# Kernel tuning notes

Hardware: AMD Instinct MI355X
Metric: run time of the kernel (lower is better)

## Reference

```python
import jax, jax.numpy as jnp
import numpy as np

BINS = np.array([1, 2, 3, 4, 8, 16, 32, 64], dtype=np.int32)


def setup_inputs() -> dict:
    N, G, F, H, K = 1024, 620, 20, 150, 128
    D_in = 3 * G + F  # 1880
    key = jax.random.key(0)
    ks = jax.random.split(key, 10)
    g = jax.random.normal(ks[0], (N, G), dtype=jnp.float32)
    si = jax.random.normal(ks[1], (N,), dtype=jnp.float32)
    i1 = jnp.sort(jax.random.randint(ks[2], (N,), 0, 8192)).astype(jnp.int32)
    i2 = jnp.sort(jax.random.randint(ks[3], (N,), 0, 8192)).astype(jnp.int32)
    dist_emb = jax.random.normal(ks[4], (9, F), dtype=jnp.float32) * 0.02
    W1 = jax.random.normal(ks[5], (D_in, H), dtype=jnp.float32) * (1.0 / np.sqrt(D_in))
    b1 = jnp.zeros((H,), jnp.float32)
    W2 = jax.random.normal(ks[6], (H, H), dtype=jnp.float32) * (1.0 / np.sqrt(H))
    b2 = jnp.zeros((H,), jnp.float32)
    W3 = jax.random.normal(ks[7], (H, 1), dtype=jnp.float32) * (1.0 / np.sqrt(H))
    b3 = jnp.zeros((1,), jnp.float32)
    return {"g": g, "si": si, "i1": i1, "i2": i2, "dist_emb": dist_emb,
            "W1": W1, "b1": b1, "W2": W2, "b2": b2, "W3": W3, "b3": b3, "K": K}


def reference(g, si, i1, i2, dist_emb, W1, b1, W2, b2, W3, b3, K):
    # Dropout is inference-disabled; epsilon dummy antecedent appended as last column.
    N, G = g.shape
    # span n's antecedents are spans [max(0, n-K), n); lay out as [N, K] window
    j_idx = jnp.arange(N)[:, None] - K + jnp.arange(K)[None, :]  # [N, K]
    valid = j_idx >= 0
    j = jnp.clip(j_idx, 0, N - 1)
    g_j = g[j]                      # [N, K, G] ragged gather (masked dense)
    g_i = g[:, None, :]             # [N, 1, G]
    # distance feature: bin(i.i2 - j.i1) with idx = #bins <= d
    d = i2[:, None] - i1[j]         # [N, K]
    bin_idx = jnp.searchsorted(jnp.asarray(BINS), d, side='right')
    de = dist_emb[bin_idx]          # [N, K, F]
    pairs = jnp.concatenate(
        [jnp.broadcast_to(g_i, (N, K, G)), g_j, g_i * g_j, de], axis=-1)  # [N, K, 3G+F]
    h = jax.nn.relu(jnp.einsum('nkd,dh->nkh', pairs, W1) + b1)
    h = jax.nn.relu(jnp.einsum('nkh,hm->nkm', h, W2) + b2)
    s = (jnp.einsum('nkh,ho->nko', h, W3) + b3)[..., 0]  # [N, K]
    sij = si[:, None] + si[j] + s
    sij = jnp.where(valid, sij, 0.0)
    eps = jnp.zeros((N, 1), sij.dtype)  # epsilon dummy score
    return jnp.concatenate([sij, eps], axis=-1)  # [N, K+1]
```

## Files before the change

kernel.cpp:

```cpp
#include <hip/hip_runtime.h>
#include <hip/hip_bf16.h>
#include <stdint.h>

typedef __attribute__((ext_vector_type(8))) short short8;
typedef __attribute__((ext_vector_type(4))) float float4_t;

#define N_PTS 1024
#define G_DIM 620
#define G_PAD 640
#define F_DIM 20
#define H_DIM 150
#define H_PAD 160
#define K_WIN 128
#define OUT_C (K_WIN + 1)

__device__ __forceinline__ float bf2f(short u) {
  union { unsigned int i; float f; } x;
  x.i = ((unsigned int)(unsigned short)u) << 16;
  return x.f;
}
__device__ __forceinline__ short f2bf(float f) {
  union { float f; unsigned int i; } x; x.f = f;
  unsigned int u = x.i;
  u += 0x7FFFu + ((u >> 16) & 1u);
  return (short)(u >> 16);
}
__device__ __forceinline__ short f2bf_hw(float f) {
  __hip_bfloat16 h = __float2bfloat16(f);
  union { __hip_bfloat16 h; short s; } u; u.h = h;
  return u.s;
}
__device__ __forceinline__ void gload_lds16(const void* g, void* l) {
  __builtin_amdgcn_global_load_lds(
      (const __attribute__((address_space(1))) unsigned int*)g,
      (__attribute__((address_space(3))) unsigned int*)l, 16, 0, 0);
}

__global__ void prep_pack(const float* __restrict__ g, const float* __restrict__ W1,
                          const float* __restrict__ W2, const float* __restrict__ dist_emb,
                          short* __restrict__ g_bf, short* __restrict__ W1cT,
                          short* __restrict__ W1abT, short* __restrict__ W2T,
                          float* __restrict__ deW) {
  __shared__ float lds[32 * 165];
  const int bx = blockIdx.x, tid = threadIdx.x;
  if (bx < 256) {
    const int n0 = bx * 4;
    for (int c = tid; c < 320; c += 256) {
      int r = c / 80, cc = c - r * 80;
      int n = n0 + r, d0 = cc * 8;
      short8 o;
      if (d0 + 8 <= G_DIM) {
        const float* src = g + n * G_DIM + d0;
        #pragma unroll
        for (int e = 0; e < 8; ++e) o[e] = f2bf(src[e]);
      } else {
        #pragma unroll
        for (int e = 0; e < 8; ++e) {
          int d = d0 + e;
          o[e] = (d < G_DIM) ? f2bf(g[n * G_DIM + d]) : (short)0;
        }
      }
      *(short8*)(g_bf + n * G_PAD + d0) = o;
    }
  } else if (bx < 316) {
    const int tb = bx - 256;
    const int third = tb / 20, dt = tb - third * 20;
    const int d0 = dt * 32;
    for (int c = tid; c < 1280; c += 256) {
      int dr = c / 40, ch4 = c - dr * 40;
      int dd = d0 + dr;
      int w1r = third * G_DIM + dd;
      #pragma unroll
      for (int e = 0; e < 4; ++e) {
        int h = ch4 * 4 + e;
        lds[dr * 165 + h] = (dd < G_DIM && h < H_DIM) ? W1[w1r * H_DIM + h] : 0.f;
      }
    }
    __syncthreads();
    short* outp = (third == 2) ? W1cT : (W1abT + third * H_PAD * G_PAD);
    for (int c = tid; c < 640; c += 256) {
      int h = c >> 2, ch = c & 3;
      short8 o;
      #pragma unroll
      for (int e = 0; e < 8; ++e) o[e] = f2bf(lds[(ch * 8 + e) * 165 + h]);
      *(short8*)(outp + h * G_PAD + d0 + ch * 8) = o;
    }
  } else if (bx < 320) {
    const int base = (bx - 316) * 6400;
    for (int c = tid; c < 6400; c += 256) {
      int q = base + c;
      int m = q / H_PAD, k = q - m * H_PAD;
      W2T[q] = (m < H_DIM && k < H_DIM) ? f2bf(W2[k * H_DIM + m]) : (short)0;
    }
  } else {
    for (int c = tid; c < 9 * H_PAD; c += 256) {
      int b = c / H_PAD, h = c - b * H_PAD;
      float acc = 0.f;
      if (h < H_DIM)
        for (int f = 0; f < F_DIM; ++f)
          acc += dist_emb[b * F_DIM + f] * W1[(3 * G_DIM + f) * H_DIM + h];
      deW[c] = acc;
    }
  }
}

__global__ __launch_bounds__(256) void prep_uv_mfma(
    const short* __restrict__ g_bf, const short* __restrict__ W1abT,
    const float* __restrict__ b1, float* __restrict__ U, float* __restrict__ V) {
  __shared__ __align__(16) char sA[32 * 128];
  __shared__ __align__(16) char sB[160 * 128];
  const int m0 = blockIdx.x * 32;
  const int yb = blockIdx.y * H_PAD;
  const int tid = threadIdx.x, lane = tid & 63, wid = tid >> 6;
  const int wm = wid >> 1, wn = wid & 1;
  const int lo4 = lane & 15, hi2 = lane >> 4;
  const int l8 = lane >> 3, c8 = lane & 7;
  const int xe = (c8 ^ (l8 & 7)) * 8;

  const float4_t fz = {0.f, 0.f, 0.f, 0.f};
  float4_t acc[5];
  #pragma unroll
  for (int b = 0; b < 5; ++b) acc[b] = fz;

  for (int step = 0; step < 10; ++step) {
    const int d0 = step * 64;
    {
      int row = wid * 8 + l8;
      gload_lds16(g_bf + (m0 + row) * G_PAD + d0 + xe, sA + (wid * 8) * 128);
    }
    #pragma unroll
    for (int cc = 0; cc < 5; ++cc) {
      int row = wid * 8 + cc * 32 + l8;
      gload_lds16(W1abT + (yb + row) * G_PAD + d0 + xe, sB + (wid * 8 + cc * 32) * 128);
    }
    __syncthreads();
    #pragma unroll
    for (int ks = 0; ks < 2; ++ks) {
      const int kb = ks * 64 + 16 * hi2;
      short8 af, bq[5];
      {
        int row = wm * 16 + lo4;
        af = *((const short8*)(sA + row * 128 + (kb ^ ((row & 7) << 4))));
      }
      #pragma unroll
      for (int nt = 0; nt < 5; ++nt) {
        int row = wn * 80 + nt * 16 + lo4;
        bq[nt] = *((const short8*)(sB + row * 128 + (kb ^ ((row & 7) << 4))));
      }
      #pragma unroll
      for (int nt = 0; nt < 5; ++nt)
        acc[nt] = __builtin_amdgcn_mfma_f32_16x16x32_bf16(af, bq[nt], acc[nt], 0, 0, 0);
    }
    __syncthreads();
  }

  const bool isU = (blockIdx.y == 0);
  float* O = isU ? U : V;
  #pragma unroll
  for (int r = 0; r < 4; ++r) {
    int m = m0 + wm * 16 + hi2 * 4 + r;
    #pragma unroll
    for (int nt = 0; nt < 5; ++nt) {
      int h = wn * 80 + nt * 16 + lo4;
      float v = acc[nt][r];
      if (h < H_DIM) { if (isU) v += b1[h]; } else { v = 0.f; }
      O[m * H_PAD + h] = v;
    }
  }
}

__global__ __launch_bounds__(512, 4) void pair_main(
    const short* __restrict__ g_bf, const short* __restrict__ W1cT,
    const short* __restrict__ W2T, const float* __restrict__ U,
    const float* __restrict__ V, const float* __restrict__ deW,
    const float* __restrict__ si, const int* __restrict__ i1,
    const int* __restrict__ i2, const float* __restrict__ W3,
    const float* __restrict__ b2, const float* __restrict__ b3,
    float* __restrict__ out) {
  __shared__ __align__(16) char smem[73728];
  __shared__ __align__(16) short gi_s[G_PAD];
  __shared__ float sj_s[K_WIN];
  __shared__ unsigned char bin_su[K_WIN];
  __shared__ float s_buf[2][K_WIN];

  char* const P0 = smem;
  char* const P1 = smem + 16384;
  char* const B0 = smem + 32768;
  char* const B1 = smem + 53248;
  char* const Hb = smem;

  const int bid = blockIdx.x;
  const int i = ((bid & 7) << 7) | (bid >> 3);
  const int tid = threadIdx.x;
  const int lane = tid & 63;
  const int wid = tid >> 6;
  const int wm = wid >> 1;
  const int wn = wid & 1;
  const int lo4 = lane & 15, hi2 = lane >> 4;
  const int l8 = lane >> 3, c8 = lane & 7;
  const int xe = (c8 ^ (l8 & 7)) * 8;
  const int tc8 = tid & 7;

  if (tid < G_PAD / 8)
    ((short8*)gi_s)[tid] = ((const short8*)(g_bf + i * G_PAD))[tid];
  if (tid < K_WIN) {
    int jr = i - K_WIN + tid, jc = jr < 0 ? 0 : jr;
    int d = i2[i] - i1[jc];
    bin_su[tid] = (unsigned char)((d >= 1) + (d >= 2) + (d >= 3) + (d >= 4) +
                                  (d >= 8) + (d >= 16) + (d >= 32) + (d >= 64));
    sj_s[tid] = si[jc];
  }
  __syncthreads();

  auto loadA = [&](int s, short8 (&gjv)[2], short8& gvv) {
    const int d0 = s * 64;
    gvv = *((const short8*)(gi_s + d0 + tc8 * 8));
    #pragma unroll
    for (int cc = 0; cc < 2; ++cc) {
      int c = tid + 512 * cc, row = c >> 3;
      int jr = i - K_WIN + row, jc = jr < 0 ? 0 : jr;
      gjv[cc] = *((const short8*)(g_bf + jc * G_PAD + d0 + tc8 * 8));
    }
  };
  auto stageB = [&](int s, char* B) {
    const int d0 = s * 64;
    #pragma unroll
    for (int cc = 0; cc < 3; ++cc) {
      if (cc < 2 || wid < 4) {
        int rowb = wid * 8 + cc * 64;
        gload_lds16(W1cT + (rowb + l8) * G_PAD + d0 + xe, B + rowb * 128);
      }
    }
  };
  auto writeP = [&](char* P, const short8 (&gjv)[2], const short8& gvv) {
    #pragma unroll
    for (int cc = 0; cc < 2; ++cc) {
      int c = tid + 512 * cc, row = c >> 3;
      short8 p;
      #pragma unroll
      for (int e = 0; e < 8; ++e) p[e] = f2bf_hw(bf2f(gjv[cc][e]) * bf2f(gvv[e]));
      int byte = row * 128 + ((tc8 * 16) ^ ((row & 7) << 4));
      *((short8*)(P + byte)) = p;
    }
  };

  {
    short8 gjv[2], gvv;
    loadA(0, gjv, gvv);
    stageB(0, B0);
    writeP(P0, gjv, gvv);
  }

  const float4_t fz = {0.f, 0.f, 0.f, 0.f};
  float4_t acc[2][5];
  #pragma unroll
  for (int a = 0; a < 2; ++a)
    #pragma unroll
    for (int b = 0; b < 5; ++b) acc[a][b] = fz;

  for (int s = 0; s < 10; ++s) {
    char* Pc = (s & 1) ? P1 : P0;
    char* Bc = (s & 1) ? B1 : B0;
    char* Pn = (s & 1) ? P0 : P1;
    char* Bn = (s & 1) ? B0 : B1;
    __syncthreads();
    short8 gjv[2], gvv;
    if (s < 9) {
      loadA(s + 1, gjv, gvv);
      stageB(s + 1, Bn);
    }
    __builtin_amdgcn_s_setprio(1);
    #pragma unroll
    for (int ks = 0; ks < 2; ++ks) {
      const int kb = ks * 64 + 16 * hi2;
      short8 af[2], bq[5];
      #pragma unroll
      for (int mt = 0; mt < 2; ++mt) {
        int row = wm * 32 + mt * 16 + lo4;
        af[mt] = *((const short8*)(Pc + row * 128 + (kb ^ ((row & 7) << 4))));
      }
      #pragma unroll
      for (int nt = 0; nt < 5; ++nt) {
        int row = wn * 80 + nt * 16 + lo4;
        bq[nt] = *((const short8*)(Bc + row * 128 + (kb ^ ((row & 7) << 4))));
      }
      #pragma unroll
      for (int mt = 0; mt < 2; ++mt)
        #pragma unroll
        for (int nt = 0; nt < 5; ++nt)
          acc[mt][nt] = __builtin_amdgcn_mfma_f32_16x16x32_bf16(af[mt], bq[nt], acc[mt][nt], 0, 0, 0);
    }
    __builtin_amdgcn_s_setprio(0);
    if (s < 9) writeP(Pn, gjv, gvv);
  }
  __syncthreads();

  float uih[5];
  #pragma unroll
  for (int nt = 0; nt < 5; ++nt) uih[nt] = U[i * H_PAD + wn * 80 + nt * 16 + lo4];
  #pragma unroll
  for (int mt = 0; mt < 2; ++mt) {
    #pragma unroll
    for (int r = 0; r < 4; ++r) {
      int m = wm * 32 + mt * 16 + hi2 * 4 + r;
      int jr = i - K_WIN + m, jc = jr < 0 ? 0 : jr;
      const float* Vj = V + jc * H_PAD;
      const float* De = deW + bin_su[m] * H_PAD;
      #pragma unroll
      for (int nt = 0; nt < 5; ++nt) {
        int h = wn * 80 + nt * 16 + lo4;
        float val = acc[mt][nt][r] + uih[nt] + Vj[h] + De[h];
        val = (h < H_DIM) ? fmaxf(val, 0.f) : 0.f;
        int tile = h >> 6, hc = h & 63;
        int byte = tile * 16384 + m * 128 + ((hc * 2) ^ ((m & 7) << 4));
        *((short*)(Hb + byte)) = f2bf_hw(val);
      }
    }
  }
  {
    short8 z = {0, 0, 0, 0, 0, 0, 0, 0};
    int c = tid;
    int row = c >> 2, cb = c & 3;
    int byte = 2 * 16384 + row * 128 + ((64 + cb * 16) ^ ((row & 7) << 4));
    *((short8*)(Hb + byte)) = z;
  }
  __syncthreads();

  float4_t acc2[2][5];
  #pragma unroll
  for (int a = 0; a < 2; ++a)
    #pragma unroll
    for (int b = 0; b < 5; ++b) acc2[a][b] = fz;

  short8 bql[2][5];
  #pragma unroll
  for (int nt = 0; nt < 5; ++nt) {
    int row = wn * 80 + nt * 16 + lo4;
    bql[0][nt] = *(const short8*)(W2T + row * H_PAD + hi2 * 8);
  }
  #pragma unroll
  for (int ks = 0; ks < 5; ++ks) {
    const int cur = ks & 1;
    if (ks < 4) {
      #pragma unroll
      for (int nt = 0; nt < 5; ++nt) {
        int row = wn * 80 + nt * 16 + lo4;
        bql[cur ^ 1][nt] = *(const short8*)(W2T + row * H_PAD + (ks + 1) * 32 + hi2 * 8);
      }
    }
    short8 af[2];
    #pragma unroll
    for (int mt = 0; mt < 2; ++mt) {
      int row = wm * 32 + mt * 16 + lo4;
      int kb = (ks & 1) * 64 + hi2 * 16;
      af[mt] = *((const short8*)(Hb + (ks >> 1) * 16384 + row * 128 + (kb ^ ((row & 7) << 4))));
    }
    __builtin_amdgcn_s_setprio(1);
    #pragma unroll
    for (int mt = 0; mt < 2; ++mt)
      #pragma unroll
      for (int nt = 0; nt < 5; ++nt)
        acc2[mt][nt] = __builtin_amdgcn_mfma_f32_16x16x32_bf16(af[mt], bql[cur][nt], acc2[mt][nt], 0, 0, 0);
    __builtin_amdgcn_s_setprio(0);
  }

  float sp[2][4];
  #pragma unroll
  for (int mt = 0; mt < 2; ++mt)
    #pragma unroll
    for (int r = 0; r < 4; ++r) sp[mt][r] = 0.f;

  #pragma unroll
  for (int nt = 0; nt < 5; ++nt) {
    int h = wn * 80 + nt * 16 + lo4;
    float w3 = (h < H_DIM) ? W3[h] : 0.f;
    float bb = (h < H_DIM) ? b2[h] : 0.f;
    #pragma unroll
    for (int mt = 0; mt < 2; ++mt)
      #pragma unroll
      for (int r = 0; r < 4; ++r) {
        float hv = fmaxf(acc2[mt][nt][r] + bb, 0.f);
        sp[mt][r] += hv * w3;
      }
  }
  #pragma unroll
  for (int mt = 0; mt < 2; ++mt)
    #pragma unroll
    for (int r = 0; r < 4; ++r) {
      float v = sp[mt][r];
      v += __shfl_xor(v, 1);
      v += __shfl_xor(v, 2);
      v += __shfl_xor(v, 4);
      v += __shfl_xor(v, 8);
      sp[mt][r] = v;
    }
  if (lo4 == 0) {
    #pragma unroll
    for (int mt = 0; mt < 2; ++mt)
      #pragma unroll
      for (int r = 0; r < 4; ++r) {
        int m = wm * 32 + mt * 16 + hi2 * 4 + r;
        s_buf[wn][m] = sp[mt][r];
      }
  }
  __syncthreads();

  if (tid < K_WIN) {
    int m = tid;
    int jr = i - K_WIN + m;
    float sij = si[i] + sj_s[m] + s_buf[0][m] + s_buf[1][m] + b3[0];
    out[i * OUT_C + m] = (jr >= 0) ? sij : 0.f;
  }
  if (tid == K_WIN) out[i * OUT_C + K_WIN] = 0.f;
}

extern "C" void kernel_launch(void* const* d_in, const int* in_sizes, int n_in,
                              void* d_out, int out_size, void* d_ws, size_t ws_size,
                              hipStream_t stream) {
  const float* g  = (const float*)d_in[0];
  const float* si = (const float*)d_in[1];
  const int*   i1 = (const int*)d_in[2];
  const int*   i2 = (const int*)d_in[3];
  const float* de = (const float*)d_in[4];
  const float* W1 = (const float*)d_in[5];
  const float* b1 = (const float*)d_in[6];
  const float* W2 = (const float*)d_in[7];
  const float* b2 = (const float*)d_in[8];
  const float* W3 = (const float*)d_in[9];
  const float* b3 = (const float*)d_in[10];
  float* out = (float*)d_out;

  char* ws = (char*)d_ws;
  short* g_bf  = (short*)(ws);
  short* W1cT  = (short*)(ws + 1310720);
  short* W1abT = (short*)(ws + 1515520);
  short* W2T   = (short*)(ws + 1925120);
  float* U     = (float*)(ws + 1976320);
  float* V     = (float*)(ws + 2631680);
  float* deW   = (float*)(ws + 3287040);

  prep_pack<<<321, 256, 0, stream>>>(g, W1, W2, de, g_bf, W1cT, W1abT, W2T, deW);
  prep_uv_mfma<<<dim3(32, 2), 256, 0, stream>>>(g_bf, W1abT, b1, U, V);
  pair_main<<<N_PTS, 512, 0, stream>>>(g_bf, W1cT, W2T, U, V, deW,
                                       si, i1, i2, W3, b2, b3, out);
}
```

Measured before the change: 72.79 us.

## Triple-buffer W1 tiles with prefetch depth two and partial vmcnt barriers

The pair_main K-loop now stages the W1c B-tile two steps ahead into three rotating LDS buffers instead of a double buffer. Each step ends with a barrier that waits on vmcnt(3) rather than draining all outstanding loads. The loop is fully unrolled, and setprio now wraps only the MFMA block. LDS use grows to about 94KB and launch bounds drop to 2 blocks per CU, trading occupancy for deeper latency hiding of global-to-LDS loads.

```diff
diff --git a/kernel.cpp b/kernel.cpp
--- a/kernel.cpp
+++ b/kernel.cpp
@@ -34,6 +34,16 @@
   __builtin_amdgcn_global_load_lds(
       (const __attribute__((address_space(1))) unsigned int*)g,
       (__attribute__((address_space(3))) unsigned int*)l, 16, 0, 0);
+}
+__device__ __forceinline__ void phase_bar3() {
+  asm volatile("s_waitcnt vmcnt(3) lgkmcnt(0)" ::: "memory");
+  __builtin_amdgcn_s_barrier();
+  __builtin_amdgcn_sched_barrier(0);
+}
+__device__ __forceinline__ void phase_bar0() {
+  asm volatile("s_waitcnt vmcnt(0) lgkmcnt(0)" ::: "memory");
+  __builtin_amdgcn_s_barrier();
+  __builtin_amdgcn_sched_barrier(0);
 }
 
 __global__ void prep_pack(const float* __restrict__ g, const float* __restrict__ W1,
@@ -169,7 +179,7 @@
   }
 }
 
-__global__ __launch_bounds__(512, 4) void pair_main(
+__global__ __launch_bounds__(512, 2) void pair_main(
     const short* __restrict__ g_bf, const short* __restrict__ W1cT,
     const short* __restrict__ W2T, const float* __restrict__ U,
     const float* __restrict__ V, const float* __restrict__ deW,
@@ -177,16 +187,17 @@
     const int* __restrict__ i2, const float* __restrict__ W3,
     const float* __restrict__ b2, const float* __restrict__ b3,
     float* __restrict__ out) {
-  __shared__ __align__(16) char smem[73728];
+  __shared__ __align__(16) char smem[94208];
   __shared__ __align__(16) short gi_s[G_PAD];
   __shared__ float sj_s[K_WIN];
   __shared__ unsigned char bin_su[K_WIN];
   __shared__ float s_buf[2][K_WIN];
 
-  char* const P0 = smem;
-  char* const P1 = smem + 16384;
-  char* const B0 = smem + 32768;
-  char* const B1 = smem + 53248;
+  char* const B0 = smem;
+  char* const B1 = smem + 20480;
+  char* const B2 = smem + 40960;
+  char* const P0 = smem + 61440;
+  char* const P1 = smem + 77824;
   char* const Hb = smem;
 
   const int bid = blockIdx.x;
@@ -244,54 +255,60 @@
     }
   };
 
+  const float4_t fz = {0.f, 0.f, 0.f, 0.f};
+  float4_t acc[2][5];
+  #pragma unroll
+  for (int a = 0; a < 2; ++a)
+    #pragma unroll
+    for (int b = 0; b < 5; ++b) acc[a][b] = fz;
+
+  auto mfma_step = [&](const char* Pc, const char* Bc) {
+    #pragma unroll
+    for (int ks = 0; ks < 2; ++ks) {
+      const int kb = ks * 64 + 16 * hi2;
+      short8 af[2], bq[5];
+      #pragma unroll
+      for (int mt = 0; mt < 2; ++mt) {
+        int row = wm * 32 + mt * 16 + lo4;
+        af[mt] = *((const short8*)(Pc + row * 128 + (kb ^ ((row & 7) << 4))));
+      }
+      #pragma unroll
+      for (int nt = 0; nt < 5; ++nt) {
+        int row = wn * 80 + nt * 16 + lo4;
+        bq[nt] = *((const short8*)(Bc + row * 128 + (kb ^ ((row & 7) << 4))));
+      }
+      __builtin_amdgcn_s_setprio(1);
+      #pragma unroll
+      for (int mt = 0; mt < 2; ++mt)
+        #pragma unroll
+        for (int nt = 0; nt < 5; ++nt)
+          acc[mt][nt] = __builtin_amdgcn_mfma_f32_16x16x32_bf16(af[mt], bq[nt], acc[mt][nt], 0, 0, 0);
+      __builtin_amdgcn_s_setprio(0);
+    }
+  };
+
   {
     short8 gjv[2], gvv;
     loadA(0, gjv, gvv);
     stageB(0, B0);
+    stageB(1, B1);
     writeP(P0, gjv, gvv);
-  }
-
-  const float4_t fz = {0.f, 0.f, 0.f, 0.f};
-  float4_t acc[2][5];
-  #pragma unroll
-  for (int a = 0; a < 2; ++a)
-    #pragma unroll
-    for (int b = 0; b < 5; ++b) acc[a][b] = fz;
-
+    phase_bar3();
+  }
+
+  char* const Bbuf[3] = {B0, B1, B2};
+  char* const Pbuf[2] = {P0, P1};
+  #pragma unroll
   for (int s = 0; s < 10; ++s) {
-    char* Pc = (s & 1) ? P1 : P0;
-    char* Bc = (s & 1) ? B1 : B0;
-    char* Pn = (s & 1) ? P0 : P1;
-    char* Bn = (s & 1) ? B0 : B1;
-    __syncthreads();
+    char* Pc = Pbuf[s & 1];
+    char* Bc = Bbuf[s % 3];
     short8 gjv[2], gvv;
-    if (s < 9) {
-      loadA(s + 1, gjv, gvv);
-      stageB(s + 1, Bn);
-    }
-    __builtin_amdgcn_s_setprio(1);
-    #pragma unroll
-    for (int ks = 0; ks < 2; ++ks) {
-      const int kb = ks * 64 + 16 * hi2;
-      short8 af[2], bq[5];
-      #pragma unroll
-      for (int mt = 0; mt < 2; ++mt) {
-        int row = wm * 32 + mt * 16 + lo4;
-        af[mt] = *((const short8*)(Pc + row * 128 + (kb ^ ((row & 7) << 4))));
-      }
-      #pragma unroll
-      for (int nt = 0; nt < 5; ++nt) {
-        int row = wn * 80 + nt * 16 + lo4;
-        bq[nt] = *((const short8*)(Bc + row * 128 + (kb ^ ((row & 7) << 4))));
-      }
-      #pragma unroll
-      for (int mt = 0; mt < 2; ++mt)
-        #pragma unroll
-        for (int nt = 0; nt < 5; ++nt)
-          acc[mt][nt] = __builtin_amdgcn_mfma_f32_16x16x32_bf16(af[mt], bq[nt], acc[mt][nt], 0, 0, 0);
-    }
-    __builtin_amdgcn_s_setprio(0);
-    if (s < 9) writeP(Pn, gjv, gvv);
+    if (s < 9) loadA(s + 1, gjv, gvv);
+    if (s < 8) stageB(s + 2, Bbuf[(s + 2) % 3]);
+    mfma_step(Pc, Bc);
+    if (s < 9) writeP(Pbuf[(s + 1) & 1], gjv, gvv);
+    if (s < 8)      phase_bar3();
+    else if (s < 9) phase_bar0();
   }
   __syncthreads();
 
```

Result: slower. 90.29 us (+24.0%).

## Use single-buffered 128-wide K tiles instead of double-buffered 64-wide tiles

Applied to the files above, without the earlier changes.

Doubles the K-step of the main GEMM loop from 64 to 128 columns, cutting the loop to 5 iterations, and replaces the double-buffered P/B LDS tiles with single buffers. It adds a second barrier per iteration and issues the W1 staging only after compute finishes. The aim is fewer barriers and iterations with the same LDS footprint. The cost is lost overlap between the async W1 loads and the MFMA work, plus more registers for the A-tile prefetch.

```diff
diff --git a/kernel.cpp b/kernel.cpp
--- a/kernel.cpp
+++ b/kernel.cpp
@@ -183,10 +183,8 @@
   __shared__ unsigned char bin_su[K_WIN];
   __shared__ float s_buf[2][K_WIN];
 
-  char* const P0 = smem;
-  char* const P1 = smem + 16384;
-  char* const B0 = smem + 32768;
-  char* const B1 = smem + 53248;
+  char* const Bb = smem;
+  char* const Pb = smem + 40960;
   char* const Hb = smem;
 
   const int bid = blockIdx.x;
@@ -197,9 +195,7 @@
   const int wm = wid >> 1;
   const int wn = wid & 1;
   const int lo4 = lane & 15, hi2 = lane >> 4;
-  const int l8 = lane >> 3, c8 = lane & 7;
-  const int xe = (c8 ^ (l8 & 7)) * 8;
-  const int tc8 = tid & 7;
+  const int tcb = tid & 15;
 
   if (tid < G_PAD / 8)
     ((short8*)gi_s)[tid] = ((const short8*)(g_bf + i * G_PAD))[tid];
@@ -212,44 +208,37 @@
   }
   __syncthreads();
 
-  auto loadA = [&](int s, short8 (&gjv)[2], short8& gvv) {
-    const int d0 = s * 64;
-    gvv = *((const short8*)(gi_s + d0 + tc8 * 8));
-    #pragma unroll
-    for (int cc = 0; cc < 2; ++cc) {
-      int c = tid + 512 * cc, row = c >> 3;
+  auto loadA = [&](int s, short8 (&gjv)[4], short8& gvv) {
+    const int d0 = s * 128;
+    gvv = *((const short8*)(gi_s + d0 + tcb * 8));
+    #pragma unroll
+    for (int cc = 0; cc < 4; ++cc) {
+      int row = (tid + 512 * cc) >> 4;
       int jr = i - K_WIN + row, jc = jr < 0 ? 0 : jr;
-      gjv[cc] = *((const short8*)(g_bf + jc * G_PAD + d0 + tc8 * 8));
+      gjv[cc] = *((const short8*)(g_bf + jc * G_PAD + d0 + tcb * 8));
     }
   };
-  auto stageB = [&](int s, char* B) {
-    const int d0 = s * 64;
-    #pragma unroll
-    for (int cc = 0; cc < 3; ++cc) {
-      if (cc < 2 || wid < 4) {
-        int rowb = wid * 8 + cc * 64;
-        gload_lds16(W1cT + (rowb + l8) * G_PAD + d0 + xe, B + rowb * 128);
-      }
+  auto stageB = [&](int s) {
+    const int d0 = s * 128;
+    #pragma unroll
+    for (int q = 0; q < 5; ++q) {
+      int rowb = (wid * 5 + q) * 4;
+      int srow = rowb + (lane >> 4);
+      int sw = ((lane & 15) ^ ((rowb & 4) | (lane >> 4))) * 8;
+      gload_lds16(W1cT + srow * G_PAD + d0 + sw, Bb + rowb * 256);
     }
   };
-  auto writeP = [&](char* P, const short8 (&gjv)[2], const short8& gvv) {
-    #pragma unroll
-    for (int cc = 0; cc < 2; ++cc) {
-      int c = tid + 512 * cc, row = c >> 3;
+  auto writeP = [&](const short8 (&gjv)[4], const short8& gvv) {
+    #pragma unroll
+    for (int cc = 0; cc < 4; ++cc) {
+      int row = (tid + 512 * cc) >> 4;
       short8 p;
       #pragma unroll
       for (int e = 0; e < 8; ++e) p[e] = f2bf_hw(bf2f(gjv[cc][e]) * bf2f(gvv[e]));
-      int byte = row * 128 + ((tc8 * 16) ^ ((row & 7) << 4));
-      *((short8*)(P + byte)) = p;
+      int byte = row * 256 + ((tcb * 16) ^ ((row & 7) << 4));
+      *((short8*)(Pb + byte)) = p;
     }
   };
-
-  {
-    short8 gjv[2], gvv;
-    loadA(0, gjv, gvv);
-    stageB(0, B0);
-    writeP(P0, gjv, gvv);
-  }
 
   const float4_t fz = {0.f, 0.f, 0.f, 0.f};
   float4_t acc[2][5];
@@ -258,31 +247,31 @@
     #pragma unroll
     for (int b = 0; b < 5; ++b) acc[a][b] = fz;
 
-  for (int s = 0; s < 10; ++s) {
-    char* Pc = (s & 1) ? P1 : P0;
-    char* Bc = (s & 1) ? B1 : B0;
-    char* Pn = (s & 1) ? P0 : P1;
-    char* Bn = (s & 1) ? B0 : B1;
+  {
+    short8 gjv[4], gvv;
+    loadA(0, gjv, gvv);
+    stageB(0);
+    writeP(gjv, gvv);
+  }
+
+  for (int s = 0; s < 5; ++s) {
     __syncthreads();
-    short8 gjv[2], gvv;
-    if (s < 9) {
-      loadA(s + 1, gjv, gvv);
-      stageB(s + 1, Bn);
-    }
+    short8 gjv[4], gvv;
+    if (s < 4) loadA(s + 1, gjv, gvv);
     __builtin_amdgcn_s_setprio(1);
     #pragma unroll
-    for (int ks = 0; ks < 2; ++ks) {
-      const int kb = ks * 64 + 16 * hi2;
+    for (int ks = 0; ks < 4; ++ks) {
+      const int kb = ks * 64 + hi2 * 16;
       short8 af[2], bq[5];
       #pragma unroll
       for (int mt = 0; mt < 2; ++mt) {
         int row = wm * 32 + mt * 16 + lo4;
-        af[mt] = *((const short8*)(Pc + row * 128 + (kb ^ ((row & 7) << 4))));
+        af[mt] = *((const short8*)(Pb + row * 256 + (kb ^ ((row & 7) << 4))));
       }
       #pragma unroll
       for (int nt = 0; nt < 5; ++nt) {
         int row = wn * 80 + nt * 16 + lo4;
-        bq[nt] = *((const short8*)(Bc + row * 128 + (kb ^ ((row & 7) << 4))));
+        bq[nt] = *((const short8*)(Bb + row * 256 + (kb ^ ((row & 7) << 4))));
       }
       #pragma unroll
       for (int mt = 0; mt < 2; ++mt)
@@ -291,9 +280,12 @@
           acc[mt][nt] = __builtin_amdgcn_mfma_f32_16x16x32_bf16(af[mt], bq[nt], acc[mt][nt], 0, 0, 0);
     }
     __builtin_amdgcn_s_setprio(0);
-    if (s < 9) writeP(Pn, gjv, gvv);
-  }
-  __syncthreads();
+    __syncthreads();
+    if (s < 4) {
+      stageB(s + 1);
+      writeP(gjv, gvv);
+    }
+  }
 
   float uih[5];
   #pragma unroll
```

After: 73.45 us. Within noise of the previous version (+0.9%).
